# Performance work log

Hardware: AMD Instinct MI355X
Metric: run time of the kernel (lower is better)

## Reference

```python
import jax, jax.numpy as jnp
import numpy as np

IN_DIM, OUT_DIM = 256, 64
N_WNODES, N_PNODES, N_EDGES = 100000, 50000, 1600000


def setup_inputs() -> dict:
    key = jax.random.key(0)
    k_h, k_src, k_dst, k_fc, k_attn = jax.random.split(key, 5)
    h = jax.random.normal(k_h, (N_WNODES, IN_DIM), dtype=jnp.float32)
    edge_src = jax.random.randint(k_src, (N_EDGES,), 0, N_WNODES)
    edge_dst = jax.random.randint(k_dst, (N_EDGES,), 0, N_PNODES)
    W_fc = jax.random.normal(k_fc, (IN_DIM, OUT_DIM), dtype=jnp.float32) / np.sqrt(IN_DIM)
    # attn_fc: Linear(2*out_dim, 1, bias=False) -> weight vector of length 2*OUT_DIM
    W_attn = jax.random.normal(k_attn, (2 * OUT_DIM,), dtype=jnp.float32) / np.sqrt(2 * OUT_DIM)
    return {"h": h, "edge_src": edge_src, "edge_dst": edge_dst,
            "n_pnodes": N_PNODES, "W_fc": W_fc, "W_attn": W_attn}


def reference(h, edge_src, edge_dst, n_pnodes, W_fc, W_attn):
    D = W_fc.shape[1]
    z = h @ W_fc                                  # [Nw, D]
    z_src = z[edge_src]                           # [E, D] gather (memory-bound)
    # In the original, only word nodes get 'z'; DGL zero-fills dst 'z', so the
    # dst half of attn_fc contributes nothing: e = leaky_relu(z_src @ a_src + 0 @ a_dst)
    a_src = W_attn[:D]
    e = jax.nn.leaky_relu(z_src @ a_src)          # [E], slope 0.01 matches torch default
    # reduce_func masks zero-valued scores (DGL mailbox padding) with -1000
    e = jnp.where(e == 0.0, -1000.0, e)
    # segment softmax over incoming edges of each destination node
    e_max = jax.ops.segment_max(e, edge_dst, num_segments=n_pnodes)
    e_max = jnp.where(jnp.isfinite(e_max), e_max, 0.0)  # guard empty segments
    w = jnp.exp(e - e_max[edge_dst])              # [E]
    denom = jax.ops.segment_sum(w, edge_dst, num_segments=n_pnodes)
    alpha = w / jnp.maximum(denom[edge_dst], 1e-20)
    # weighted gather-scatter aggregation: sh[dst] = sum alpha * z_src
    h_out = jax.ops.segment_sum(alpha[:, None] * z_src, edge_dst, num_segments=n_pnodes)
    return h_out                                  # [n_pnodes, D] == h[pnode_id]
```

## Files before the change

### kernel.cpp

```cpp
#include <hip/hip_runtime.h>
#include <hip/hip_bf16.h>
#include <math.h>

#define IN_DIM 256
#define OUT_DIM 64
#define CHUNK_LOG2 12
#define BK_LOG2 7
#define MAXNB 512
#define BCAP 6144

typedef __attribute__((ext_vector_type(8))) short short8v;
typedef __attribute__((ext_vector_type(4))) float f32x4;

__device__ __forceinline__ unsigned short f2bf(float f) {
    unsigned u = __float_as_uint(f);
    unsigned r = (u + 0x7fffu + ((u >> 16) & 1u)) >> 16;
    return (unsigned short)r;
}

__device__ __forceinline__ float bf2f(unsigned short b) {
    return __uint_as_float(((unsigned)b) << 16);
}

__device__ __forceinline__ float edge_score(float x) {
    float e = x > 0.0f ? x : 0.01f * x;
    if (e == 0.0f) e = -1000.0f;
    return e;
}

__device__ __forceinline__ void gload_lds16(const void* g, void* l) {
    __builtin_amdgcn_global_load_lds(
        (const __attribute__((address_space(1))) unsigned int*)g,
        (__attribute__((address_space(3))) unsigned int*)l, 16, 0, 0);
}

__global__ __launch_bounds__(256) void prep_kernel(
    const float* __restrict__ Wfc, short8v* __restrict__ wtf)
{
    const int v = blockIdx.x * 256 + threadIdx.x;
    const int ks = v >> 8;
    const int t = (v >> 6) & 3;
    const int lane = v & 63;
    const int lg = lane >> 4, lr = lane & 15;
    short8v b;
    #pragma unroll
    for (int j = 0; j < 8; ++j) {
        const int k = ks * 32 + lg * 8 + j;
        b[j] = (short)f2bf(Wfc[k * OUT_DIM + t * 16 + lr]);
    }
    wtf[v] = b;
}

__global__ __launch_bounds__(256, 2) void gemm_s_kernel(
    const float* __restrict__ h, const short8v* __restrict__ wtf,
    const float* __restrict__ Wattn, unsigned short* __restrict__ z,
    float* __restrict__ s, int n_rows)
{
    __shared__ float hl[64 * IN_DIM];
    const int tid = threadIdx.x;
    const int lane = tid & 63;
    const int wv = tid >> 6;
    const int lg = lane >> 4;
    const int lr = lane & 15;
    const int row0 = blockIdx.x * 64;

    short8v Bf[8][4];
    #pragma unroll
    for (int ks = 0; ks < 8; ++ks)
        #pragma unroll
        for (int t = 0; t < 4; ++t)
            Bf[ks][t] = wtf[(ks * 4 + t) * 64 + lane];

    float a_attn[4];
    #pragma unroll
    for (int t = 0; t < 4; ++t) a_attn[t] = Wattn[t * 16 + lr];

    #pragma unroll
    for (int i = 0; i < 16; ++i) {
        const int q = i * 256 + tid;
        const int row = q >> 6;
        const int within = q & 63;
        const int lslot = within ^ (row & 7);
        const int grow = min(row0 + row, n_rows - 1);
        gload_lds16(h + (size_t)grow * IN_DIM + lslot * 4, hl + q * 4);
    }
    __syncthreads();

    f32x4 acc[4];
    #pragma unroll
    for (int t = 0; t < 4; ++t) acc[t] = (f32x4){0.f, 0.f, 0.f, 0.f};

    const int rowl = wv * 16 + lr;
    const char* rbase = (const char*)hl + rowl * 1024;
    const int swz = (lr & 7) << 4;

    union AB { short8v v; __hip_bfloat162 h2[4]; };
    #pragma unroll
    for (int ks = 0; ks < 8; ++ks) {
        const int lb = ks * 128 + lg * 32;
        const float4 x0 = *(const float4*)(rbase + (lb ^ swz));
        const float4 x1 = *(const float4*)(rbase + ((lb + 16) ^ swz));
        AB u;
        u.h2[0] = __float22bfloat162_rn(float2{x0.x, x0.y});
        u.h2[1] = __float22bfloat162_rn(float2{x0.z, x0.w});
        u.h2[2] = __float22bfloat162_rn(float2{x1.x, x1.y});
        u.h2[3] = __float22bfloat162_rn(float2{x1.z, x1.w});
        #pragma unroll
        for (int t = 0; t < 4; ++t)
            acc[t] = __builtin_amdgcn_mfma_f32_16x16x32_bf16(u.v, Bf[ks][t], acc[t], 0, 0, 0);
    }

    #pragma unroll
    for (int j = 0; j < 4; ++j) {
        const int row = row0 + wv * 16 + lg * 4 + j;
        const bool ok = row < n_rows;
        float sv = 0.0f;
        #pragma unroll
        for (int t = 0; t < 4; ++t) {
            const float v = acc[t][j];
            if (ok) z[(size_t)row * OUT_DIM + t * 16 + lr] =
                __bfloat16_as_ushort(__float2bfloat16(v));
            sv = fmaf(v, a_attn[t], sv);
        }
        #pragma unroll
        for (int o = 1; o < 16; o <<= 1) sv += __shfl_xor(sv, o);
        if (ok && lr == 0) s[row] = sv;
    }
}

__global__ __launch_bounds__(512) void scatter_kernel(
    const int* __restrict__ esrc, const int* __restrict__ edst,
    int* __restrict__ bres, int* __restrict__ brec, int n_edges, int nb)
{
    __shared__ int lcnt[MAXNB];
    __shared__ int lwoff[MAXNB];
    const int tid = threadIdx.x;
    const int i0 = blockIdx.x << CHUNK_LOG2;
    const int i1 = min(i0 + (1 << CHUNK_LOG2), n_edges);
    const bool full = (i1 - i0) == (1 << CHUNK_LOG2);

    int4 s4[2], d4[2];
    if (full) {
        const int4* sp = (const int4*)esrc + (i0 >> 2);
        const int4* dp = (const int4*)edst + (i0 >> 2);
        s4[0] = sp[tid];       s4[1] = sp[512 + tid];
        d4[0] = dp[tid];       d4[1] = dp[512 + tid];
    }

    for (int j = tid; j < nb; j += 512) lcnt[j] = 0;
    __syncthreads();
    if (full) {
        #pragma unroll
        for (int j = 0; j < 2; ++j) {
            atomicAdd(&lcnt[d4[j].x >> BK_LOG2], 1);
            atomicAdd(&lcnt[d4[j].y >> BK_LOG2], 1);
            atomicAdd(&lcnt[d4[j].z >> BK_LOG2], 1);
            atomicAdd(&lcnt[d4[j].w >> BK_LOG2], 1);
        }
    } else {
        for (int i = i0 + tid; i < i1; i += 512)
            atomicAdd(&lcnt[edst[i] >> BK_LOG2], 1);
    }
    __syncthreads();
    for (int j = tid; j < nb; j += 512) {
        const int cv = lcnt[j];
        lwoff[j] = cv ? (j * BCAP + atomicAdd(bres + j, cv)) : 0;
    }
    __syncthreads();
    if (full) {
        #pragma unroll
        for (int j = 0; j < 2; ++j) {
            #define EMIT(dd, ss) { \
                const int pos = atomicAdd(&lwoff[(dd) >> BK_LOG2], 1); \
                brec[pos] = (ss) | (((dd) & ((1 << BK_LOG2) - 1)) << 17); }
            EMIT(d4[j].x, s4[j].x)
            EMIT(d4[j].y, s4[j].y)
            EMIT(d4[j].z, s4[j].z)
            EMIT(d4[j].w, s4[j].w)
            #undef EMIT
        }
    } else {
        for (int i = i0 + tid; i < i1; i += 512) {
            const int d = edst[i];
            const int pos = atomicAdd(&lwoff[d >> BK_LOG2], 1);
            brec[pos] = esrc[i] | ((d & ((1 << BK_LOG2) - 1)) << 17);
        }
    }
}

__global__ __launch_bounds__(256) void p2_kernel(
    const int* __restrict__ bres, int* __restrict__ brec,
    int2* __restrict__ oln, int n_pnodes)
{
    __shared__ int srec[BCAP];
    __shared__ int lh[128], lsc[128], lwf[128];
    const int b = blockIdx.x;
    const int tid = threadIdx.x;
    const int base = b * BCAP;
    const int len = min(bres[b], BCAP);

    if (tid < 128) lh[tid] = 0;
    __syncthreads();
    for (int i = tid; i < len; i += 256) {
        const int r = brec[base + i];
        srec[i] = r;
        atomicAdd(&lh[r >> 17], 1);
    }
    __syncthreads();
    if (tid < 128) lsc[tid] = lh[tid];
    __syncthreads();
    for (int d = 1; d < 128; d <<= 1) {
        int v = 0;
        if (tid < 128 && tid >= d) v = lsc[tid - d];
        __syncthreads();
        if (tid < 128) lsc[tid] += v;
        __syncthreads();
    }
    const int d0 = b << BK_LOG2;
    if (tid < 128) {
        const int st = lsc[tid] - lh[tid];
        lwf[tid] = st;
        if (d0 + tid < n_pnodes)
            oln[d0 + tid] = make_int2(base + st, lh[tid]);
    }
    __syncthreads();
    for (int i = tid; i < len; i += 256) {
        const int r = srec[i];
        const int pos = atomicAdd(&lwf[r >> 17], 1);
        brec[base + pos] = r & 0x1FFFF;
    }
}

__global__ __launch_bounds__(256) void segment_kernel(
    const int2* __restrict__ oln, const int* __restrict__ ssrc,
    const float* __restrict__ s, const unsigned short* __restrict__ z,
    float* __restrict__ out, int n_pnodes)
{
    const int p = blockIdx.x * 4 + (threadIdx.x >> 6);
    if (p >= n_pnodes) return;
    const int lane = threadIdx.x & 63;
    const int2 ol = oln[p];
    const int beg = ol.x;
    const int len = ol.y;
    const int end = beg + len;

    if (len == 0) {
        out[(size_t)p * OUT_DIM + lane] = 0.0f;
        return;
    }

    float acc = 0.0f, dsum = 0.0f;

    #define GATH1(tt, wsrc, ssrcv) { \
        float wt = __shfl(wsrc, tt); \
        int st = __shfl(ssrcv, tt); \
        acc = fmaf(wt, bf2f(z[(size_t)st * OUT_DIM + lane]), acc); }
    #define GATH8(tt, wsrc, ssrcv) { \
        float w0 = __shfl(wsrc, tt),     w1 = __shfl(wsrc, tt + 1); \
        float w2 = __shfl(wsrc, tt + 2), w3 = __shfl(wsrc, tt + 3); \
        float w4 = __shfl(wsrc, tt + 4), w5 = __shfl(wsrc, tt + 5); \
        float w6 = __shfl(wsrc, tt + 6), w7 = __shfl(wsrc, tt + 7); \
        int a0 = __shfl(ssrcv, tt),     a1 = __shfl(ssrcv, tt + 1); \
        int a2 = __shfl(ssrcv, tt + 2), a3 = __shfl(ssrcv, tt + 3); \
        int a4 = __shfl(ssrcv, tt + 4), a5 = __shfl(ssrcv, tt + 5); \
        int a6 = __shfl(ssrcv, tt + 6), a7 = __shfl(ssrcv, tt + 7); \
        float z0 = bf2f(z[(size_t)a0 * OUT_DIM + lane]); \
        float z1 = bf2f(z[(size_t)a1 * OUT_DIM + lane]); \
        float z2 = bf2f(z[(size_t)a2 * OUT_DIM + lane]); \
        float z3 = bf2f(z[(size_t)a3 * OUT_DIM + lane]); \
        float z4 = bf2f(z[(size_t)a4 * OUT_DIM + lane]); \
        float z5 = bf2f(z[(size_t)a5 * OUT_DIM + lane]); \
        float z6 = bf2f(z[(size_t)a6 * OUT_DIM + lane]); \
        float z7 = bf2f(z[(size_t)a7 * OUT_DIM + lane]); \
        acc = fmaf(w0, z0, acc); acc = fmaf(w1, z1, acc); \
        acc = fmaf(w2, z2, acc); acc = fmaf(w3, z3, acc); \
        acc = fmaf(w4, z4, acc); acc = fmaf(w5, z5, acc); \
        acc = fmaf(w6, z6, acc); acc = fmaf(w7, z7, acc); }

    if (len <= 64) {
        const bool v = lane < len;
        const int j = beg + (v ? lane : 0);
        const int sr = ssrc[j];
        const float e = v ? edge_score(s[sr]) : -INFINITY;
        float m = e;
        #pragma unroll
        for (int o = 32; o > 0; o >>= 1) m = fmaxf(m, __shfl_xor(m, o));
        float w = v ? __expf(e - m) : 0.0f;
        dsum = w;
        #pragma unroll
        for (int o = 32; o > 0; o >>= 1) dsum += __shfl_xor(dsum, o);

        int t = 0;
        for (; t + 8 <= len; t += 8) GATH8(t, w, sr)
        for (; t < len; ++t) GATH1(t, w, sr)
    } else {
        float m = -INFINITY;
        for (int j = beg + lane; j < end; j += 64)
            m = fmaxf(m, edge_score(s[ssrc[j]]));
        #pragma unroll
        for (int o = 32; o > 0; o >>= 1) m = fmaxf(m, __shfl_xor(m, o));

        for (int c = beg; c < end; c += 64) {
            const int j = c + lane;
            float w = 0.0f;
            int sr = 0;
            if (j < end) {
                sr = ssrc[j];
                w = __expf(edge_score(s[sr]) - m);
            }
            dsum += w;
            const int cn = min(64, end - c);
            int t = 0;
            for (; t + 8 <= cn; t += 8) GATH8(t, w, sr)
            for (; t < cn; ++t) GATH1(t, w, sr)
        }
        #pragma unroll
        for (int o = 32; o > 0; o >>= 1) dsum += __shfl_xor(dsum, o);
    }
    #undef GATH8
    #undef GATH1

    out[(size_t)p * OUT_DIM + lane] = acc / fmaxf(dsum, 1e-20f);
}

extern "C" void kernel_launch(void* const* d_in, const int* in_sizes, int n_in,
                              void* d_out, int out_size, void* d_ws, size_t ws_size,
                              hipStream_t stream)
{
    const float* h     = (const float*)d_in[0];
    const int*   esrc  = (const int*)d_in[1];
    const int*   edst  = (const int*)d_in[2];
    const float* Wfc   = (const float*)d_in[4];
    const float* Wattn = (const float*)d_in[5];
    float* out = (float*)d_out;

    const int n_w = in_sizes[0] / IN_DIM;
    const int n_e = in_sizes[1];
    const int n_p = out_size / OUT_DIM;
    const int nb  = (n_p + (1 << BK_LOG2) - 1) >> BK_LOG2;

    short8v* wtf            = (short8v*)d_ws;
    unsigned short* z       = (unsigned short*)(wtf + 2048);
    float* s                = (float*)(z + (size_t)n_w * OUT_DIM);
    int* brec               = (int*)(s + n_w);
    int2* oln               = (int2*)(brec + (size_t)nb * BCAP);
    int* bres               = (int*)(oln + n_p);

    hipMemsetAsync(bres, 0, (size_t)nb * sizeof(int), stream);

    prep_kernel<<<8, 256, 0, stream>>>(Wfc, wtf);
    const int gemm_blocks = (n_w + 63) / 64;
    gemm_s_kernel<<<gemm_blocks, 256, 0, stream>>>(h, wtf, Wattn, z, s, n_w);

    const int nchunks = (n_e + (1 << CHUNK_LOG2) - 1) >> CHUNK_LOG2;
    scatter_kernel<<<nchunks, 512, 0, stream>>>(esrc, edst, bres, brec, n_e, nb);
    p2_kernel<<<nb, 256, 0, stream>>>(bres, brec, oln, n_p);
    segment_kernel<<<(n_p + 3) / 4, 256, 0, stream>>>(oln, brec, s, z, out, n_p);
}
```

Measured before the change: 117.7 us.

## Fuse edge scatter and GEMM into one launch with block-range dispatch

Merges the edge bucketing scatter kernel and the dense GEMM/score kernel into a single launch. The first nchunks blocks do the scatter, now with 256 threads handling 4 int4 loads each and reusing the GEMM's shared buffer for counters, and the remaining blocks run the GEMM. The aim is to overlap the memory/atomic-bound scatter with the GEMM and drop one launch boundary. The cost is that scatter blocks inherit the GEMM's large shared-memory footprint and register budget, which may limit how many scatter blocks are resident at once.

New measurement: 110.8 us. 5.8% less time.

```diff
diff --git a/kernel.cpp b/kernel.cpp
--- a/kernel.cpp
+++ b/kernel.cpp
@@ -51,18 +51,83 @@
     wtf[v] = b;
 }
 
-__global__ __launch_bounds__(256, 2) void gemm_s_kernel(
+__global__ __launch_bounds__(256, 2) void mega_kernel(
     const float* __restrict__ h, const short8v* __restrict__ wtf,
-    const float* __restrict__ Wattn, unsigned short* __restrict__ z,
-    float* __restrict__ s, int n_rows)
+    const float* __restrict__ Wattn, const int* __restrict__ esrc,
+    const int* __restrict__ edst, unsigned short* __restrict__ z,
+    float* __restrict__ s, int* __restrict__ bres, int* __restrict__ brec,
+    int n_rows, int n_edges, int nb, int nchunks)
 {
     __shared__ float hl[64 * IN_DIM];
+    const int bid = blockIdx.x;
     const int tid = threadIdx.x;
+
+    if (bid < nchunks) {
+        int* lcnt = (int*)hl;
+        int* lwoff = lcnt + MAXNB;
+        const int i0 = bid << CHUNK_LOG2;
+        const int i1 = min(i0 + (1 << CHUNK_LOG2), n_edges);
+        const bool full = (i1 - i0) == (1 << CHUNK_LOG2);
+
+        int4 s4[4], d4[4];
+        if (full) {
+            const int4* sp = (const int4*)esrc + (i0 >> 2);
+            const int4* dp = (const int4*)edst + (i0 >> 2);
+            #pragma unroll
+            for (int j = 0; j < 4; ++j) {
+                s4[j] = sp[j * 256 + tid];
+                d4[j] = dp[j * 256 + tid];
+            }
+        }
+
+        for (int j = tid; j < nb; j += 256) lcnt[j] = 0;
+        __syncthreads();
+        if (full) {
+            #pragma unroll
+            for (int j = 0; j < 4; ++j) {
+                atomicAdd(&lcnt[d4[j].x >> BK_LOG2], 1);
+                atomicAdd(&lcnt[d4[j].y >> BK_LOG2], 1);
+                atomicAdd(&lcnt[d4[j].z >> BK_LOG2], 1);
+                atomicAdd(&lcnt[d4[j].w >> BK_LOG2], 1);
+            }
+        } else {
+            for (int i = i0 + tid; i < i1; i += 256)
+                atomicAdd(&lcnt[edst[i] >> BK_LOG2], 1);
+        }
+        __syncthreads();
+        for (int j = tid; j < nb; j += 256) {
+            const int cv = lcnt[j];
+            lwoff[j] = cv ? (j * BCAP + atomicAdd(bres + j, cv)) : 0;
+        }
+        __syncthreads();
+        if (full) {
+            #pragma unroll
+            for (int j = 0; j < 4; ++j) {
+                #define EMIT(dd, ss) { \
+                    const int pos = atomicAdd(&lwoff[(dd) >> BK_LOG2], 1); \
+                    brec[pos] = (ss) | (((dd) & ((1 << BK_LOG2) - 1)) << 17); }
+                EMIT(d4[j].x, s4[j].x)
+                EMIT(d4[j].y, s4[j].y)
+                EMIT(d4[j].z, s4[j].z)
+                EMIT(d4[j].w, s4[j].w)
+                #undef EMIT
+            }
+        } else {
+            for (int i = i0 + tid; i < i1; i += 256) {
+                const int d = edst[i];
+                const int pos = atomicAdd(&lwoff[d >> BK_LOG2], 1);
+                brec[pos] = esrc[i] | ((d & ((1 << BK_LOG2) - 1)) << 17);
+            }
+        }
+        return;
+    }
+
+    const int gb = bid - nchunks;
     const int lane = tid & 63;
     const int wv = tid >> 6;
     const int lg = lane >> 4;
     const int lr = lane & 15;
-    const int row0 = blockIdx.x * 64;
+    const int row0 = gb * 64;
 
     short8v Bf[8][4];
     #pragma unroll
@@ -125,66 +190,6 @@
         #pragma unroll
         for (int o = 1; o < 16; o <<= 1) sv += __shfl_xor(sv, o);
         if (ok && lr == 0) s[row] = sv;
-    }
-}
-
-__global__ __launch_bounds__(512) void scatter_kernel(
-    const int* __restrict__ esrc, const int* __restrict__ edst,
-    int* __restrict__ bres, int* __restrict__ brec, int n_edges, int nb)
-{
-    __shared__ int lcnt[MAXNB];
-    __shared__ int lwoff[MAXNB];
-    const int tid = threadIdx.x;
-    const int i0 = blockIdx.x << CHUNK_LOG2;
-    const int i1 = min(i0 + (1 << CHUNK_LOG2), n_edges);
-    const bool full = (i1 - i0) == (1 << CHUNK_LOG2);
-
-    int4 s4[2], d4[2];
-    if (full) {
-        const int4* sp = (const int4*)esrc + (i0 >> 2);
-        const int4* dp = (const int4*)edst + (i0 >> 2);
-        s4[0] = sp[tid];       s4[1] = sp[512 + tid];
-        d4[0] = dp[tid];       d4[1] = dp[512 + tid];
-    }
-
-    for (int j = tid; j < nb; j += 512) lcnt[j] = 0;
-    __syncthreads();
-    if (full) {
-        #pragma unroll
-        for (int j = 0; j < 2; ++j) {
-            atomicAdd(&lcnt[d4[j].x >> BK_LOG2], 1);
-            atomicAdd(&lcnt[d4[j].y >> BK_LOG2], 1);
-            atomicAdd(&lcnt[d4[j].z >> BK_LOG2], 1);
-            atomicAdd(&lcnt[d4[j].w >> BK_LOG2], 1);
-        }
-    } else {
-        for (int i = i0 + tid; i < i1; i += 512)
-            atomicAdd(&lcnt[edst[i] >> BK_LOG2], 1);
-    }
-    __syncthreads();
-    for (int j = tid; j < nb; j += 512) {
-        const int cv = lcnt[j];
-        lwoff[j] = cv ? (j * BCAP + atomicAdd(bres + j, cv)) : 0;
-    }
-    __syncthreads();
-    if (full) {
-        #pragma unroll
-        for (int j = 0; j < 2; ++j) {
-            #define EMIT(dd, ss) { \
-                const int pos = atomicAdd(&lwoff[(dd) >> BK_LOG2], 1); \
-                brec[pos] = (ss) | (((dd) & ((1 << BK_LOG2) - 1)) << 17); }
-            EMIT(d4[j].x, s4[j].x)
-            EMIT(d4[j].y, s4[j].y)
-            EMIT(d4[j].z, s4[j].z)
-            EMIT(d4[j].w, s4[j].w)
-            #undef EMIT
-        }
-    } else {
-        for (int i = i0 + tid; i < i1; i += 512) {
-            const int d = edst[i];
-            const int pos = atomicAdd(&lwoff[d >> BK_LOG2], 1);
-            brec[pos] = esrc[i] | ((d & ((1 << BK_LOG2) - 1)) << 17);
-        }
     }
 }
 
@@ -349,11 +354,12 @@
     hipMemsetAsync(bres, 0, (size_t)nb * sizeof(int), stream);
 
     prep_kernel<<<8, 256, 0, stream>>>(Wfc, wtf);
-    const int gemm_blocks = (n_w + 63) / 64;
-    gemm_s_kernel<<<gemm_blocks, 256, 0, stream>>>(h, wtf, Wattn, z, s, n_w);
 
     const int nchunks = (n_e + (1 << CHUNK_LOG2) - 1) >> CHUNK_LOG2;
-    scatter_kernel<<<nchunks, 512, 0, stream>>>(esrc, edst, bres, brec, n_e, nb);
+    const int gemmb = (n_w + 63) / 64;
+    mega_kernel<<<nchunks + gemmb, 256, 0, stream>>>(h, wtf, Wattn, esrc, edst,
+                                                     z, s, bres, brec,
+                                                     n_w, n_e, nb, nchunks);
     p2_kernel<<<nb, 256, 0, stream>>>(bres, brec, oln, n_p);
     segment_kernel<<<(n_p + 3) / 4, 256, 0, stream>>>(oln, brec, s, z, out, n_p);
 }
```
